# Kernel tuning notes

Hardware: AMD Instinct MI355X
Metric: run time of the kernel (lower is better)

The kernel has to match this reference:

```python
import jax, jax.numpy as jnp
import numpy as np

B, T, E, C, H = 8, 96, 96, 256, 8
D = C // H
HID = int(C * 4.0)
EPS = 1e-5


def _ln(x, g, b):
    m = x.mean(-1, keepdims=True)
    v = ((x - m) ** 2).mean(-1, keepdims=True)
    return (x - m) * jax.lax.rsqrt(v + EPS) * g + b


def setup_inputs() -> dict:
    key = jax.random.key(0)
    ks = jax.random.split(key, 20)
    s = 0.02
    inp = {
        "x": jax.random.normal(ks[0], (B, T, E, C), jnp.float32),
        "adj_mask": jax.random.uniform(ks[1], (E, E), jnp.float32) * 2.0 - 1.0,  # direction cosines in [-1,1]
        "n1_g": jnp.ones((C,)), "n1_b": jnp.zeros((C,)),
        "s_wq": jax.random.normal(ks[2], (C, C)) * s,
        "s_wk": jax.random.normal(ks[3], (C, C)) * s,
        "s_wv": jax.random.normal(ks[4], (C, C)) * s,
        "s_wp": jax.random.normal(ks[5], (C, C)) * s,
        "s_bp": jnp.zeros((C,)),
        "s_ng": jnp.ones((C,)), "s_nb": jnp.zeros((C,)),
        "s_gamma": jax.random.normal(ks[6], (1,)) * 0.1,
        "n2_g": jnp.ones((C,)), "n2_b": jnp.zeros((C,)),
        "t_wq": jax.random.normal(ks[7], (C, C)) * s,
        "t_wk": jax.random.normal(ks[8], (C, C)) * s,
        "t_wv": jax.random.normal(ks[9], (C, C)) * s,
        "t_wp": jax.random.normal(ks[10], (C, C)) * s,
        "t_bp": jnp.zeros((C,)),
        "t_gamma": jax.random.normal(ks[11], (1,)) * 0.1,
        "n3_g": jnp.ones((C,)), "n3_b": jnp.zeros((C,)),
        "m_w1": jax.random.normal(ks[12], (C, HID)) * s,
        "m_b1": jnp.zeros((HID,)),
        "m_w2": jax.random.normal(ks[13], (HID, C)) * s,
        "m_b2": jnp.zeros((C,)),
    }
    return inp


def _interp_linear_T(x, t_new):
    # x: [B, T, E, C]; torch F.interpolate(mode='linear', align_corners=False) over T
    t = x.shape[1]
    scale = t / t_new
    src = (jnp.arange(t_new, dtype=jnp.float32) + 0.5) * scale - 0.5
    src = jnp.clip(src, 0.0, t - 1)
    i0 = jnp.floor(src).astype(jnp.int32)
    i1 = jnp.minimum(i0 + 1, t - 1)
    w = (src - i0.astype(jnp.float32))[None, :, None, None]
    return x[:, i0] * (1.0 - w) + x[:, i1] * w


def reference(x, adj_mask, n1_g, n1_b, s_wq, s_wk, s_wv, s_wp, s_bp, s_ng, s_nb, s_gamma,
              n2_g, n2_b, t_wq, t_wk, t_wv, t_wp, t_bp, t_gamma,
              n3_g, n3_b, m_w1, m_b1, m_w2, m_b2):
    b, t, e, c = x.shape
    h, d = H, C // H

    # ---- spatial geometric-cosine attention (per frame) ----
    xs = _ln(x, n1_g, n1_b)                                    # identity inside spatial_attn
    q = (xs @ s_wq).reshape(b, t, e, h, d)
    k = (xs @ s_wk).reshape(b, t, e, h, d)
    v = (xs @ s_wv).reshape(b, t, e, h, d)
    attn = jnp.einsum('btqhd,btkhd->bthqk', q, k)
    attn = (attn * adj_mask + 1.0) * 0.5                        # masked-cosine, no softmax
    o = jnp.einsum('bthqk,btkhd->btqhd', attn, v).reshape(b, t, e, c)
    o = _ln(o @ s_wp + s_bp, s_ng, s_nb)
    x = x + (xs + s_gamma * o)

    # ---- temporal softmax attention (per edge) ----
    xt = _ln(x, n2_g, n2_b)
    q = (xt @ t_wq).reshape(b, t, e, h, d)
    k = (xt @ t_wk).reshape(b, t, e, h, d)
    v = (xt @ t_wv).reshape(b, t, e, h, d)
    attn = jnp.einsum('bqehd,bkehd->behqk', q, k) * (d ** -0.5)
    attn = jax.nn.softmax(attn, axis=-1)
    o = jnp.einsum('behqk,bkehd->bqehd', attn, v).reshape(b, t, e, c)
    o = o @ t_wp + t_bp
    x = x + t_gamma * o

    # ---- MLP ----
    xm = _ln(x, n3_g, n3_b)
    x = x + (jax.nn.gelu(xm @ m_w1 + m_b1, approximate=False) @ m_w2 + m_b2)

    # ---- temporal downsampling (interpolate) ----
    t_new = t // 2 + t % 2
    if t > 1:
        x = _interp_linear_T(x, t_new)
    return x
```

## Files before the change

### kernel.cpp

```cpp
#include <hip/hip_runtime.h>
#include <cmath>

constexpr int BB = 8, TT = 96, EE = 96, CC = 256, HHD = 8, DDm = 32;
constexpr int NTOK = BB * TT * EE;
constexpr int TOUT = TT / 2;

typedef unsigned short u16;
typedef short bf16x8 __attribute__((ext_vector_type(8)));
typedef float f32x4 __attribute__((ext_vector_type(4)));

__device__ __forceinline__ float bf2f(u16 u) {
  union { unsigned int i; float f; } v; v.i = ((unsigned int)u) << 16; return v.f;
}
__device__ __forceinline__ u16 f2bf(float f) {
  union { unsigned int i; float f; } v; v.f = f;
  return (u16)((v.i + 0x7FFFu + ((v.i >> 16) & 1u)) >> 16);
}
__device__ __forceinline__ float wsum(float v) {
#pragma unroll
  for (int off = 32; off; off >>= 1) v += __shfl_xor(v, off);
  return v;
}
__device__ __forceinline__ float gelu_f(float x) {
  return 0.5f * x * (1.0f + erff(x * 0.70710678118654752f));
}
__device__ __forceinline__ int remap_row(int row, int mode) {
  if (mode == 0) return row;
  int b = row / (TT * EE);
  int rem = row - b * (TT * EE);
  if (mode == 1) { int t = rem / EE, e = rem - t * EE; return (b * EE + e) * TT + t; }
  int e = rem / TT, t = rem - e * TT;
  return (b * TT + t) * EE + e;
}

struct WPtr8 { const float* p[8]; };
__global__ void k_transpose8(WPtr8 src, u16* __restrict__ dst) {
  const float* in = src.p[blockIdx.y];
  u16* out = dst + (size_t)blockIdx.y * 65536;
  int idx = blockIdx.x * 256 + threadIdx.x;
  int k = idx >> 8, c = idx & 255;
  out[c * 256 + k] = f2bf(in[idx]);
}

__global__ void k_transpose(const float* __restrict__ in, u16* __restrict__ out, int K, int Nc, int n) {
  int idx = blockIdx.x * 256 + threadIdx.x;
  if (idx < n) {
    int k = idx / Nc, c = idx - k * Nc;
    out[c * K + k] = f2bf(in[idx]);
  }
}

__global__ void k_cvt(const float* __restrict__ in, u16* __restrict__ out, int n) {
  int idx = blockIdx.x * 256 + threadIdx.x;
  if (idx < n) out[idx] = f2bf(in[idx]);
}

__global__ __launch_bounds__(256) void k_ln_in(const float* __restrict__ x,
                                               u16* __restrict__ A, const float* __restrict__ g,
                                               const float* __restrict__ b) {
  int wv = threadIdx.x >> 6, lane = threadIdx.x & 63;
  long tok = (long)blockIdx.x * 4 + wv;
  int c = lane * 4;
  long off = tok * CC + c;
  float4 v = *(const float4*)(x + off);
  float s = v.x + v.y + v.z + v.w;
  float sq = v.x * v.x + v.y * v.y + v.z * v.z + v.w * v.w;
  s = wsum(s); sq = wsum(sq);
  float m = s * (1.0f / CC);
  float rs = rsqrtf(sq * (1.0f / CC) - m * m + 1e-5f);
  float4 gv = *(const float4*)(g + c);
  float4 bv = *(const float4*)(b + c);
  ushort4 o;
  o.x = f2bf((v.x - m) * rs * gv.x + bv.x);
  o.y = f2bf((v.y - m) * rs * gv.y + bv.y);
  o.z = f2bf((v.z - m) * rs * gv.z + bv.z);
  o.w = f2bf((v.w - m) * rs * gv.w + bv.w);
  *(ushort4*)(A + off) = o;
}

__global__ __launch_bounds__(256) void k_ln_f32(const float* __restrict__ X, u16* __restrict__ A,
                                                const float* __restrict__ g, const float* __restrict__ b) {
  int wv = threadIdx.x >> 6, lane = threadIdx.x & 63;
  long tok = (long)blockIdx.x * 4 + wv;
  int c = lane * 4;
  long off = tok * CC + c;
  float4 v = *(const float4*)(X + off);
  float s = v.x + v.y + v.z + v.w;
  float sq = v.x * v.x + v.y * v.y + v.z * v.z + v.w * v.w;
  s = wsum(s); sq = wsum(sq);
  float m = s * (1.0f / CC);
  float rs = rsqrtf(sq * (1.0f / CC) - m * m + 1e-5f);
  float4 gv = *(const float4*)(g + c);
  float4 bv = *(const float4*)(b + c);
  ushort4 o;
  o.x = f2bf((v.x - m) * rs * gv.x + bv.x);
  o.y = f2bf((v.y - m) * rs * gv.y + bv.y);
  o.z = f2bf((v.z - m) * rs * gv.z + bv.z);
  o.w = f2bf((v.w - m) * rs * gv.w + bv.w);
  *(ushort4*)(A + off) = o;
}

__global__ __launch_bounds__(256) void k_sp_combine(const float* __restrict__ xin, float* __restrict__ X,
                                                    u16* __restrict__ A, const u16* __restrict__ P,
                                                    const float* __restrict__ n1g, const float* __restrict__ n1b,
                                                    const float* __restrict__ sg,
                                                    const float* __restrict__ s_ng, const float* __restrict__ s_nb,
                                                    const float* __restrict__ n2g, const float* __restrict__ n2b) {
  int wv = threadIdx.x >> 6, lane = threadIdx.x & 63;
  long tok = (long)blockIdx.x * 4 + wv;
  int c = lane * 4;
  long off = tok * CC + c;
  float4 xv = *(const float4*)(xin + off);
  float s1 = xv.x + xv.y + xv.z + xv.w;
  float q1 = xv.x * xv.x + xv.y * xv.y + xv.z * xv.z + xv.w * xv.w;
  s1 = wsum(s1); q1 = wsum(q1);
  float m1 = s1 * (1.0f / CC);
  float r1 = rsqrtf(q1 * (1.0f / CC) - m1 * m1 + 1e-5f);
  float4 g1 = *(const float4*)(n1g + c);
  float4 b1 = *(const float4*)(n1b + c);
  float xs0 = (xv.x - m1) * r1 * g1.x + b1.x;
  float xs1 = (xv.y - m1) * r1 * g1.y + b1.y;
  float xs2 = (xv.z - m1) * r1 * g1.z + b1.z;
  float xs3 = (xv.w - m1) * r1 * g1.w + b1.w;
  ushort4 up = *(const ushort4*)(P + off);
  float4 p = make_float4(bf2f(up.x), bf2f(up.y), bf2f(up.z), bf2f(up.w));
  float s = p.x + p.y + p.z + p.w;
  float sq = p.x * p.x + p.y * p.y + p.z * p.z + p.w * p.w;
  s = wsum(s); sq = wsum(sq);
  float m = s * (1.0f / CC);
  float rs = rsqrtf(sq * (1.0f / CC) - m * m + 1e-5f);
  float4 ug = *(const float4*)(s_ng + c);
  float4 ub = *(const float4*)(s_nb + c);
  float o0 = (p.x - m) * rs * ug.x + ub.x;
  float o1 = (p.y - m) * rs * ug.y + ub.y;
  float o2 = (p.z - m) * rs * ug.z + ub.z;
  float o3 = (p.w - m) * rs * ug.w + ub.w;
  float gsg = sg[0];
  float x0 = xv.x + xs0 + gsg * o0;
  float x1 = xv.y + xs1 + gsg * o1;
  float x2 = xv.z + xs2 + gsg * o2;
  float x3 = xv.w + xs3 + gsg * o3;
  *(float4*)(X + off) = make_float4(x0, x1, x2, x3);
  float s2 = x0 + x1 + x2 + x3;
  float sq2 = x0 * x0 + x1 * x1 + x2 * x2 + x3 * x3;
  s2 = wsum(s2); sq2 = wsum(sq2);
  float m2 = s2 * (1.0f / CC);
  float rs2 = rsqrtf(sq2 * (1.0f / CC) - m2 * m2 + 1e-5f);
  float4 g2 = *(const float4*)(n2g + c);
  float4 b2 = *(const float4*)(n2b + c);
  ushort4 o;
  o.x = f2bf((x0 - m2) * rs2 * g2.x + b2.x);
  o.y = f2bf((x1 - m2) * rs2 * g2.y + b2.y);
  o.z = f2bf((x2 - m2) * rs2 * g2.z + b2.z);
  o.w = f2bf((x3 - m2) * rs2 * g2.w + b2.w);
  *(ushort4*)(A + off) = o;
}

__global__ __launch_bounds__(256) void k_gemm128(const u16* __restrict__ act, const u16* __restrict__ Wt,
                                                 const float* __restrict__ bias, const float* __restrict__ gptr,
                                                 u16* __restrict__ outB, float* __restrict__ Xacc,
                                                 int Kd, int Nc, int lda, int ldb, int epi, int remap) {
  __shared__ __align__(16) u16 smem[128 * 136];
  u16* As = smem;
  u16* Bs = smem + 4096;
  int m0 = blockIdx.y * 128, n0 = blockIdx.x * 128;
  int tid = threadIdx.x;
  int wv = tid >> 6, lane = tid & 63, lm = lane & 15, quad = lane >> 4;
  int wr = wv >> 1, wc = wv & 1;
  f32x4 acc[4][4];
#pragma unroll
  for (int i = 0; i < 4; i++)
#pragma unroll
    for (int j = 0; j < 4; j++) acc[i][j] = (f32x4){0.f, 0.f, 0.f, 0.f};

  for (int kk = 0; kk < Kd; kk += 32) {
#pragma unroll
    for (int j = 0; j < 2; j++) {
      int cid = j * 256 + wv * 64 + lane;
      int row = cid >> 2, seg = cid & 3;
      const u16* ga = act + (long)(m0 + row) * lda + kk + seg * 8;
      const u16* gb = Wt + (long)(n0 + row) * ldb + kk + seg * 8;
      u16* la = &As[(j * 256 + wv * 64) * 8];
      u16* lb = &Bs[(j * 256 + wv * 64) * 8];
      __builtin_amdgcn_global_load_lds(ga, la, 16, 0, 0);
      __builtin_amdgcn_global_load_lds(gb, lb, 16, 0, 0);
    }
    __syncthreads();
    bf16x8 af[4], bfv[4];
#pragma unroll
    for (int t = 0; t < 4; t++) {
      af[t] = *(const bf16x8*)&As[(wr * 64 + t * 16 + lm) * 32 + quad * 8];
      bfv[t] = *(const bf16x8*)&Bs[(wc * 64 + t * 16 + lm) * 32 + quad * 8];
    }
#pragma unroll
    for (int ti = 0; ti < 4; ti++)
#pragma unroll
      for (int tj = 0; tj < 4; tj++)
        acc[ti][tj] = __builtin_amdgcn_mfma_f32_16x16x32_bf16(af[ti], bfv[tj], acc[ti][tj], 0, 0, 0);
    __syncthreads();
  }

  if (epi == 3) {
    float gm = gptr ? gptr[0] : 1.0f;
#pragma unroll
    for (int tj = 0; tj < 4; tj++) {
      int col = n0 + wc * 64 + tj * 16 + lm;
      float bv = bias ? bias[col] : 0.0f;
#pragma unroll
      for (int ti = 0; ti < 4; ti++)
#pragma unroll
        for (int r = 0; r < 4; r++) {
          int row = remap_row(m0 + wr * 64 + ti * 16 + quad * 4 + r, remap);
          Xacc[(long)row * Nc + col] += gm * (acc[ti][tj][r] + bv);
        }
    }
  } else {
#pragma unroll
    for (int tj = 0; tj < 4; tj++) {
      int col = wc * 64 + tj * 16 + lm;
      float bv = (epi >= 1 && bias) ? bias[n0 + col] : 0.0f;
#pragma unroll
      for (int ti = 0; ti < 4; ti++)
#pragma unroll
        for (int r = 0; r < 4; r++) {
          float vv = acc[ti][tj][r] + bv;
          if (epi == 2) vv = gelu_f(vv);
          smem[(wr * 64 + ti * 16 + quad * 4 + r) * 136 + col] = f2bf(vv);
        }
    }
    __syncthreads();
#pragma unroll
    for (int p = 0; p < 8; p++) {
      int idx = p * 256 + tid;
      int row = idx >> 4, c8 = idx & 15;
      int grow = remap_row(m0 + row, remap);
      *(uint4*)(outB + (long)grow * Nc + n0 + c8 * 8) = *(const uint4*)&smem[row * 136 + c8 * 8];
    }
  }
}

__global__ __launch_bounds__(384) void k_sp_attn(const u16* __restrict__ QKV, const u16* __restrict__ adj,
                                                 u16* __restrict__ O) {
  __shared__ __align__(16) u16 Qs[96 * 32];
  __shared__ __align__(16) u16 Ks[96 * 32];
  __shared__ __align__(16) u16 Vs[96 * 32];
  __shared__ __align__(16) u16 Ss[96 * 96];
  int blk = blockIdx.x;
  int h = blk & 7, t = (blk >> 3) % TT, b = blk / (8 * TT);
  long base = ((long)(b * TT + t) * EE) * 768 + h * DDm;
  int tid = threadIdx.x;
  {
    int row = tid >> 2, seg = tid & 3;
    long goff = base + (long)row * 768 + seg * 8;
    *(uint4*)&Qs[row * 32 + seg * 8] = *(const uint4*)(QKV + goff);
    *(uint4*)&Ks[row * 32 + seg * 8] = *(const uint4*)(QKV + goff + 256);
    *(uint4*)&Vs[row * 32 + seg * 8] = *(const uint4*)(QKV + goff + 512);
#pragma unroll
    for (int i = 0; i < 3; i++) {
      int off = tid * 24 + i * 8;
      *(uint4*)&Ss[off] = *(const uint4*)(adj + off);
    }
  }
  __syncthreads();
  int wv = tid >> 6, lane = tid & 63, lm = lane & 15, quad = lane >> 4;
  bf16x8 aq = *(const bf16x8*)&Qs[(wv * 16 + lm) * 32 + quad * 8];
  f32x4 sc[6];
#pragma unroll
  for (int j = 0; j < 6; j++) {
    bf16x8 bk = *(const bf16x8*)&Ks[(j * 16 + lm) * 32 + quad * 8];
    f32x4 z = (f32x4){0.f, 0.f, 0.f, 0.f};
    sc[j] = __builtin_amdgcn_mfma_f32_16x16x32_bf16(aq, bk, z, 0, 0, 0);
  }
  u16 sv[6][4];
#pragma unroll
  for (int j = 0; j < 6; j++) {
    int col = j * 16 + lm;
#pragma unroll
    for (int r = 0; r < 4; r++) {
      int row = wv * 16 + quad * 4 + r;
      float a = bf2f(Ss[row * 96 + col]);
      sv[j][r] = f2bf((sc[j][r] * a + 1.0f) * 0.5f);
    }
  }
  __syncthreads();
#pragma unroll
  for (int j = 0; j < 6; j++) {
    int col = j * 16 + lm;
#pragma unroll
    for (int r = 0; r < 4; r++) Ss[(wv * 16 + quad * 4 + r) * 96 + col] = sv[j][r];
  }
  __syncthreads();
  f32x4 oc[2];
  oc[0] = (f32x4){0.f, 0.f, 0.f, 0.f};
  oc[1] = (f32x4){0.f, 0.f, 0.f, 0.f};
#pragma unroll
  for (int ks = 0; ks < 3; ks++) {
    bf16x8 as = *(const bf16x8*)&Ss[(wv * 16 + lm) * 96 + ks * 32 + quad * 8];
#pragma unroll
    for (int n = 0; n < 2; n++) {
      bf16x8 bv;
#pragma unroll
      for (int jj = 0; jj < 8; jj++)
        bv[jj] = (short)Vs[(ks * 32 + quad * 8 + jj) * 32 + n * 16 + lm];
      oc[n] = __builtin_amdgcn_mfma_f32_16x16x32_bf16(as, bv, oc[n], 0, 0, 0);
    }
  }
  long obase = ((long)(b * TT + t) * EE) * CC + h * DDm;
#pragma unroll
  for (int n = 0; n < 2; n++)
#pragma unroll
    for (int r = 0; r < 4; r++) {
      int row = wv * 16 + quad * 4 + r;
      O[obase + (long)row * CC + n * 16 + lm] = f2bf(oc[n][r]);
    }
}

__global__ __launch_bounds__(384) void k_tp_attn(const u16* __restrict__ QKV, u16* __restrict__ O) {
  __shared__ __align__(16) u16 Qs[96 * 32];
  __shared__ __align__(16) u16 Ks[96 * 32];
  __shared__ __align__(16) u16 Vs[96 * 32];
  __shared__ __align__(16) u16 Ss[96 * 96];
  int blk = blockIdx.x;
  int h = blk & 7, e = (blk >> 3) % EE, b = blk / (8 * EE);
  long base = ((long)(b * EE + e) * TT) * 768 + h * DDm;
  int tid = threadIdx.x;
  {
    int row = tid >> 2, seg = tid & 3;
    long goff = base + (long)row * 768 + seg * 8;
    *(uint4*)&Qs[row * 32 + seg * 8] = *(const uint4*)(QKV + goff);
    *(uint4*)&Ks[row * 32 + seg * 8] = *(const uint4*)(QKV + goff + 256);
    *(uint4*)&Vs[row * 32 + seg * 8] = *(const uint4*)(QKV + goff + 512);
  }
  __syncthreads();
  int wv = tid >> 6, lane = tid & 63, lm = lane & 15, quad = lane >> 4;
  bf16x8 aq = *(const bf16x8*)&Qs[(wv * 16 + lm) * 32 + quad * 8];
  f32x4 sc[6];
#pragma unroll
  for (int j = 0; j < 6; j++) {
    bf16x8 bk = *(const bf16x8*)&Ks[(j * 16 + lm) * 32 + quad * 8];
    f32x4 z = (f32x4){0.f, 0.f, 0.f, 0.f};
    sc[j] = __builtin_amdgcn_mfma_f32_16x16x32_bf16(aq, bk, z, 0, 0, 0);
  }
  const float scale = 0.17677669529663687f;
#pragma unroll
  for (int r = 0; r < 4; r++) {
    float mx = -1e30f;
#pragma unroll
    for (int j = 0; j < 6; j++) { sc[j][r] *= scale; mx = fmaxf(mx, sc[j][r]); }
#pragma unroll
    for (int mask = 1; mask < 16; mask <<= 1) mx = fmaxf(mx, __shfl_xor(mx, mask));
    float sum = 0.f;
#pragma unroll
    for (int j = 0; j < 6; j++) { float p = __expf(sc[j][r] - mx); sc[j][r] = p; sum += p; }
#pragma unroll
    for (int mask = 1; mask < 16; mask <<= 1) sum += __shfl_xor(sum, mask);
    float inv = 1.0f / sum;
#pragma unroll
    for (int j = 0; j < 6; j++) sc[j][r] *= inv;
  }
#pragma unroll
  for (int j = 0; j < 6; j++) {
    int col = j * 16 + lm;
#pragma unroll
    for (int r = 0; r < 4; r++) Ss[(wv * 16 + quad * 4 + r) * 96 + col] = f2bf(sc[j][r]);
  }
  __syncthreads();
  f32x4 oc[2];
  oc[0] = (f32x4){0.f, 0.f, 0.f, 0.f};
  oc[1] = (f32x4){0.f, 0.f, 0.f, 0.f};
#pragma unroll
  for (int ks = 0; ks < 3; ks++) {
    bf16x8 as = *(const bf16x8*)&Ss[(wv * 16 + lm) * 96 + ks * 32 + quad * 8];
#pragma unroll
    for (int n = 0; n < 2; n++) {
      bf16x8 bv;
#pragma unroll
      for (int jj = 0; jj < 8; jj++)
        bv[jj] = (short)Vs[(ks * 32 + quad * 8 + jj) * 32 + n * 16 + lm];
      oc[n] = __builtin_amdgcn_mfma_f32_16x16x32_bf16(as, bv, oc[n], 0, 0, 0);
    }
  }
  long obase = ((long)(b * EE + e) * TT) * CC + h * DDm;
#pragma unroll
  for (int n = 0; n < 2; n++)
#pragma unroll
    for (int r = 0; r < 4; r++) {
      int row = wv * 16 + quad * 4 + r;
      O[obase + (long)row * CC + n * 16 + lm] = f2bf(oc[n][r]);
    }
}

__global__ __launch_bounds__(256) void k_down(const float* __restrict__ X, float* __restrict__ out) {
  long i4 = ((long)blockIdx.x * 256 + threadIdx.x) * 4;
  long tmp = i4;
  int c = (int)(tmp & 255); tmp >>= 8;
  int e = (int)(tmp % EE); tmp /= EE;
  int i = (int)(tmp % TOUT);
  int b = (int)(tmp / TOUT);
  long src0 = (((long)b * TT + 2 * i) * EE + e) * CC + c;
  float4 a = *(const float4*)(X + src0);
  float4 bb = *(const float4*)(X + src0 + (long)EE * CC);
  float4 o = make_float4(0.5f * (a.x + bb.x), 0.5f * (a.y + bb.y),
                         0.5f * (a.z + bb.z), 0.5f * (a.w + bb.w));
  *(float4*)(out + i4) = o;
}

extern "C" void kernel_launch(void* const* d_in, const int* in_sizes, int n_in,
                              void* d_out, int out_size, void* d_ws, size_t ws_size,
                              hipStream_t stream) {
  (void)in_sizes; (void)n_in; (void)out_size; (void)ws_size;
  const float* x   = (const float*)d_in[0];
  const float* adj = (const float*)d_in[1];
  const float* n1g = (const float*)d_in[2];
  const float* n1b = (const float*)d_in[3];
  const float* swq = (const float*)d_in[4];
  const float* swk = (const float*)d_in[5];
  const float* swv = (const float*)d_in[6];
  const float* swp = (const float*)d_in[7];
  const float* sbp = (const float*)d_in[8];
  const float* sng = (const float*)d_in[9];
  const float* snb = (const float*)d_in[10];
  const float* sg  = (const float*)d_in[11];
  const float* n2g = (const float*)d_in[12];
  const float* n2b = (const float*)d_in[13];
  const float* twq = (const float*)d_in[14];
  const float* twk = (const float*)d_in[15];
  const float* twv = (const float*)d_in[16];
  const float* twp = (const float*)d_in[17];
  const float* tbp = (const float*)d_in[18];
  const float* tg  = (const float*)d_in[19];
  const float* n3g = (const float*)d_in[20];
  const float* n3b = (const float*)d_in[21];
  const float* mw1 = (const float*)d_in[22];
  const float* mb1 = (const float*)d_in[23];
  const float* mw2 = (const float*)d_in[24];
  const float* mb2 = (const float*)d_in[25];
  float* out = (float*)d_out;

  size_t nc = (size_t)NTOK * CC;
  float* X  = (float*)d_ws;
  u16* A    = (u16*)(X + nc);
  u16* QKV  = A + nc;
  u16* Pb   = QKV;
  u16* Hh   = QKV;
  u16* wts  = QKV + 3 * nc;
  u16* swq_t = wts;
  u16* swp_t = wts + 3 * 65536;
  u16* twq_t = wts + 4 * 65536;
  u16* twp_t = wts + 7 * 65536;
  u16* w1_t  = wts + 8 * 65536;
  u16* w2_t  = w1_t + 262144;
  u16* adj_b = w2_t + 262144;

  WPtr8 w8; w8.p[0] = swq; w8.p[1] = swk; w8.p[2] = swv; w8.p[3] = swp;
  w8.p[4] = twq; w8.p[5] = twk; w8.p[6] = twv; w8.p[7] = twp;
  k_transpose8<<<dim3(256, 8), 256, 0, stream>>>(w8, wts);
  k_transpose<<<(256 * 1024 + 255) / 256, 256, 0, stream>>>(mw1, w1_t, 256, 1024, 256 * 1024);
  k_transpose<<<(1024 * 256 + 255) / 256, 256, 0, stream>>>(mw2, w2_t, 1024, 256, 1024 * 256);
  k_cvt<<<(EE * EE + 255) / 256, 256, 0, stream>>>(adj, adj_b, EE * EE);

  auto gemm = [&](const u16* act, const u16* Wt, const float* bias, const float* gamma,
                  u16* outB, float* Xacc, int Kd, int Nc, int lda, int ldb, int epi, int remap, int M) {
    dim3 g(Nc / 128, M / 128);
    k_gemm128<<<g, 256, 0, stream>>>(act, Wt, bias, gamma, outB, Xacc, Kd, Nc, lda, ldb, epi, remap);
  };

  int lnBlocks = NTOK / 4;

  k_ln_in<<<lnBlocks, 256, 0, stream>>>(x, A, n1g, n1b);
  gemm(A, swq_t, nullptr, nullptr, QKV, nullptr, 256, 768, 256, 256, 0, 0, NTOK);
  k_sp_attn<<<BB * TT * HHD, 384, 0, stream>>>(QKV, adj_b, A);
  gemm(A, swp_t, sbp, nullptr, Pb, nullptr, 256, 256, 256, 256, 1, 0, NTOK);
  k_sp_combine<<<lnBlocks, 256, 0, stream>>>(x, X, A, Pb, n1g, n1b, sg, sng, snb, n2g, n2b);

  gemm(A, twq_t, nullptr, nullptr, QKV, nullptr, 256, 768, 256, 256, 0, 1, NTOK);
  k_tp_attn<<<BB * EE * HHD, 384, 0, stream>>>(QKV, A);
  gemm(A, twp_t, tbp, tg, nullptr, X, 256, 256, 256, 256, 3, 2, NTOK);

  k_ln_f32<<<lnBlocks, 256, 0, stream>>>(X, A, n3g, n3b);
  for (int hf = 0; hf < 2; hf++) {
    long r0 = (long)hf * (NTOK / 2);
    gemm(A + r0 * CC, w1_t, mb1, nullptr, Hh, nullptr, 256, 1024, 256, 256, 2, 0, NTOK / 2);
    gemm(Hh, w2_t, mb2, nullptr, nullptr, X + r0 * CC, 1024, 256, 1024, 1024, 3, 0, NTOK / 2);
  }

  long outElems = (long)BB * TOUT * EE * CC;
  k_down<<<(int)(outElems / 4 / 256), 256, 0, stream>>>(X, out);
}
```

Measured before the change: 810.7 us.

## Double-buffer GEMM K loop, remap workgroups per XCD, stage residual epilogue through LDS

The GEMM kernel now double-buffers its A/B tiles in shared memory, issuing the next K-slice's global-to-LDS loads before computing on the current one, with explicit waitcnt and barrier calls in place of two __syncthreads per step. Block indices in the GEMM and both attention kernels are permuted so consecutive logical tiles land on the same XCD, which is meant to improve L2 locality on the multi-die GPU. The residual-accumulate epilogue now writes into LDS first and then does coalesced float4 read-modify-write on the fp32 residual, instead of scattered scalar updates. The risks are extra barriers in the epilogue and reliance on hand-placed waitcnts for correctness.

```diff
diff --git a/kernel.cpp b/kernel.cpp
--- a/kernel.cpp
+++ b/kernel.cpp
@@ -161,9 +161,11 @@
                                                  u16* __restrict__ outB, float* __restrict__ Xacc,
                                                  int Kd, int Nc, int lda, int ldb, int epi, int remap) {
   __shared__ __align__(16) u16 smem[128 * 136];
-  u16* As = smem;
-  u16* Bs = smem + 4096;
-  int m0 = blockIdx.y * 128, n0 = blockIdx.x * 128;
+  int gx = gridDim.x;
+  int nwg = gx * gridDim.y;
+  int lid = blockIdx.y * gx + blockIdx.x;
+  if ((nwg & 7) == 0) lid = (lid & 7) * (nwg >> 3) + (lid >> 3);
+  int m0 = (lid / gx) * 128, n0 = (lid % gx) * 128;
   int tid = threadIdx.x;
   int wv = tid >> 6, lane = tid & 63, lm = lane & 15, quad = lane >> 4;
   int wr = wv >> 1, wc = wv & 1;
@@ -173,46 +175,75 @@
 #pragma unroll
     for (int j = 0; j < 4; j++) acc[i][j] = (f32x4){0.f, 0.f, 0.f, 0.f};
 
-  for (int kk = 0; kk < Kd; kk += 32) {
+  const u16* pa = act + (long)(m0 + (tid >> 2)) * lda + (tid & 3) * 8;
+  const u16* pb = Wt + (long)(n0 + (tid >> 2)) * ldb + (tid & 3) * 8;
+
+  auto STAGE = [&](int buf, int kk) {
+    u16* sb = smem + buf * 8192;
 #pragma unroll
     for (int j = 0; j < 2; j++) {
-      int cid = j * 256 + wv * 64 + lane;
-      int row = cid >> 2, seg = cid & 3;
-      const u16* ga = act + (long)(m0 + row) * lda + kk + seg * 8;
-      const u16* gb = Wt + (long)(n0 + row) * ldb + kk + seg * 8;
-      u16* la = &As[(j * 256 + wv * 64) * 8];
-      u16* lb = &Bs[(j * 256 + wv * 64) * 8];
-      __builtin_amdgcn_global_load_lds(ga, la, 16, 0, 0);
-      __builtin_amdgcn_global_load_lds(gb, lb, 16, 0, 0);
-    }
-    __syncthreads();
+      __builtin_amdgcn_global_load_lds(pa + (long)j * 64 * lda + kk, sb + (j * 256 + wv * 64) * 8, 16, 0, 0);
+      __builtin_amdgcn_global_load_lds(pb + (long)j * 64 * ldb + kk, sb + 4096 + (j * 256 + wv * 64) * 8, 16, 0, 0);
+    }
+  };
+
+  STAGE(0, 0);
+  asm volatile("s_waitcnt vmcnt(0)" ::: "memory");
+  __builtin_amdgcn_s_barrier();
+
+  int nsteps = Kd >> 5;
+  int cur = 0;
+  for (int t = 0; t < nsteps; ++t) {
+    if (t + 1 < nsteps) STAGE(cur ^ 1, (t + 1) << 5);
+    const u16* As = smem + cur * 8192;
+    const u16* Bs = As + 4096;
     bf16x8 af[4], bfv[4];
 #pragma unroll
-    for (int t = 0; t < 4; t++) {
-      af[t] = *(const bf16x8*)&As[(wr * 64 + t * 16 + lm) * 32 + quad * 8];
-      bfv[t] = *(const bf16x8*)&Bs[(wc * 64 + t * 16 + lm) * 32 + quad * 8];
+    for (int q = 0; q < 4; q++) {
+      af[q] = *(const bf16x8*)&As[(wr * 64 + q * 16 + lm) * 32 + quad * 8];
+      bfv[q] = *(const bf16x8*)&Bs[(wc * 64 + q * 16 + lm) * 32 + quad * 8];
     }
 #pragma unroll
     for (int ti = 0; ti < 4; ti++)
 #pragma unroll
       for (int tj = 0; tj < 4; tj++)
         acc[ti][tj] = __builtin_amdgcn_mfma_f32_16x16x32_bf16(af[ti], bfv[tj], acc[ti][tj], 0, 0, 0);
-    __syncthreads();
+    asm volatile("s_waitcnt lgkmcnt(0)" ::: "memory");
+    if (t + 1 < nsteps) asm volatile("s_waitcnt vmcnt(0)" ::: "memory");
+    __builtin_amdgcn_s_barrier();
+    cur ^= 1;
   }
 
   if (epi == 3) {
     float gm = gptr ? gptr[0] : 1.0f;
-#pragma unroll
-    for (int tj = 0; tj < 4; tj++) {
-      int col = n0 + wc * 64 + tj * 16 + lm;
-      float bv = bias ? bias[col] : 0.0f;
-#pragma unroll
-      for (int ti = 0; ti < 4; ti++)
-#pragma unroll
-        for (int r = 0; r < 4; r++) {
-          int row = remap_row(m0 + wr * 64 + ti * 16 + quad * 4 + r, remap);
-          Xacc[(long)row * Nc + col] += gm * (acc[ti][tj][r] + bv);
+    float* fs = (float*)smem;
+#pragma unroll
+    for (int half = 0; half < 2; half++) {
+      if (half) __syncthreads();
+      if (wr == half) {
+#pragma unroll
+        for (int tj = 0; tj < 4; tj++) {
+          int col = wc * 64 + tj * 16 + lm;
+          float bv = bias ? bias[n0 + col] : 0.0f;
+#pragma unroll
+          for (int ti = 0; ti < 4; ti++)
+#pragma unroll
+            for (int r = 0; r < 4; r++)
+              fs[(ti * 16 + quad * 4 + r) * 132 + col] = gm * (acc[ti][tj][r] + bv);
         }
+      }
+      __syncthreads();
+#pragma unroll
+      for (int p = 0; p < 8; p++) {
+        int idx = p * 256 + tid;
+        int row = idx >> 5, c4 = idx & 31;
+        int grow = remap_row(m0 + half * 64 + row, remap);
+        float* gp = Xacc + (long)grow * Nc + n0 + c4 * 4;
+        float4 xv = *(float4*)gp;
+        float4 sv = *(const float4*)&fs[row * 132 + c4 * 4];
+        xv.x += sv.x; xv.y += sv.y; xv.z += sv.z; xv.w += sv.w;
+        *(float4*)gp = xv;
+      }
     }
   } else {
 #pragma unroll
@@ -246,6 +277,7 @@
   __shared__ __align__(16) u16 Vs[96 * 32];
   __shared__ __align__(16) u16 Ss[96 * 96];
   int blk = blockIdx.x;
+  blk = (blk & 7) * ((int)gridDim.x >> 3) + (blk >> 3);
   int h = blk & 7, t = (blk >> 3) % TT, b = blk / (8 * TT);
   long base = ((long)(b * TT + t) * EE) * 768 + h * DDm;
   int tid = threadIdx.x;
@@ -321,6 +353,7 @@
   __shared__ __align__(16) u16 Vs[96 * 32];
   __shared__ __align__(16) u16 Ss[96 * 96];
   int blk = blockIdx.x;
+  blk = (blk & 7) * ((int)gridDim.x >> 3) + (blk >> 3);
   int h = blk & 7, e = (blk >> 3) % EE, b = blk / (8 * EE);
   long base = ((long)(b * EE + e) * TT) * 768 + h * DDm;
   int tid = threadIdx.x;
```

Result: faster. 698.0 us (-13.9%).
